# Performance work log

Hardware: AMD Instinct MI355X
Metric: run time of the kernel (lower is better)

Reference implementation:

```python
import jax, jax.numpy as jnp
import numpy as np

KERNEL_SIZE = 10
LEVELS = 4
PAD = (KERNEL_SIZE - 2) // 2  # 4


def _antireflect_pad(x, p):
    # antireflect: reflect around boundary value with sign flip: 2*edge - reflected interior
    left = 2.0 * x[..., :1] - x[..., 1:p + 1][..., ::-1]
    right = 2.0 * x[..., -1:] - x[..., -p - 1:-1][..., ::-1]
    return jnp.concatenate([left, x, right], axis=-1)


def _dwconv(x, kern, c):
    # depthwise grouped conv1d, stride 2, VALID (padding done explicitly)
    return jax.lax.conv_general_dilated(
        x, kern, window_strides=(2,), padding='VALID',
        feature_group_count=c, dimension_numbers=('NCH', 'OIH', 'NCH'))


def setup_inputs() -> dict:
    key = jax.random.key(0)
    k1, k2 = jax.random.split(key)
    signal = jax.random.normal(k1, (8, 64, 65536), dtype=jnp.float32)
    scaling_kernel = jax.random.normal(k2, (1, 1, KERNEL_SIZE), dtype=jnp.float32) * 0.3
    return {"signal": signal, "scaling_kernel": scaling_kernel}


def reference(signal, scaling_kernel):
    b, c, _ = signal.shape
    h = scaling_kernel  # [1,1,K]
    sign = (-1.0) ** jnp.arange(KERNEL_SIZE, dtype=signal.dtype)
    g = h[..., ::-1] * sign  # quadrature-mirror wavelet filter
    H = jnp.tile(h, (c, 1, 1))  # [C,1,K] depthwise kernels
    G = jnp.tile(g, (c, 1, 1))
    signals, details = [], []
    x = signal
    for _ in range(LEVELS):
        xp = _antireflect_pad(x, PAD)
        a = _dwconv(xp, H, c)  # approximation (normalize_approximation=False -> /1)
        d = _dwconv(xp, G, c)  # detail
        signals.append(a)
        details.append(d)
        x = jax.lax.stop_gradient(a)  # torch .detach() between levels
    return tuple(signals) + tuple(details)
```

## Files before the change

### kernel.cpp

```cpp
#include <hip/hip_runtime.h>

#define KS 10
#define NT 256
#define W  512

#define ARENA 1168

#define FENCE() asm volatile("s_waitcnt lgkmcnt(0)" ::: "memory")

struct OutPtrs { float* a[4]; float* d[4]; };

template<int EXT, int PADO, int OWN, bool TO_LDS>
__device__ __forceinline__ void wave_level(const float* __restrict__ sIn,
                                           float* __restrict__ sOut,
                                           const float* h,
                                           float* __restrict__ aRow,
                                           float* __restrict__ dRow,
                                           int obase, int lane)
{
    constexpr int ITERS = (EXT + 63) / 64;
#pragma unroll
    for (int i = 0; i < ITERS; ++i) {
        const int t = lane + 64 * i;
        if ((EXT % 64 == 0) || (t < EXT)) {
            float aa = 0.0f, dd = 0.0f;
#pragma unroll
            for (int k = 0; k < KS; ++k) {
                const float xv = sIn[2 * t + k];
                aa = fmaf(xv, h[k], aa);
                dd = fmaf(xv, (k & 1) ? -h[KS - 1 - k] : h[KS - 1 - k], dd);
            }
            if (TO_LDS) sOut[t] = aa;
            const int rel = t - PADO;
            if (rel >= 0 && rel < OWN) {
                aRow[obase + rel] = aa;
                dRow[obase + rel] = dd;
            }
        }
    }
}

__device__ __forceinline__ void patchL(float* s, int P, int lane) {
    if (lane < P) s[lane] = 2.0f * s[P] - s[2 * P - lane];
}
__device__ __forceinline__ void patchR(float* s, int P, int E, int lane) {
    if (lane < P) { const int t = E + 1 + lane; s[t] = 2.0f * s[E] - s[2 * E - t]; }
}

__global__ __launch_bounds__(NT) void dwt_wave_kernel(
    const float* __restrict__ x, const float* __restrict__ hptr, OutPtrs op, int L0)
{
    const int tid  = threadIdx.x;
    const int lane = tid & 63;
    const int wv   = tid >> 6;
    const int row  = blockIdx.y;
    const int nc   = L0 / W;
    const int c    = blockIdx.x * (NT / 64) + wv;
    const bool left  = (c == 0);
    const bool right = (c == nc - 1);

    __shared__ __align__(16) float arena[(NT / 64) * ARENA];
    float* sw  = arena + wv * ARENA;
    float* sx  = sw;
    float* sa1 = sx  + 632;
    float* sa2 = sa1 + 312;
    float* sa3 = sa2 + 152;

    float h[KS];
#pragma unroll
    for (int k = 0; k < KS; ++k) h[k] = hptr[k];

    const int L1 = L0 >> 1, L2 = L0 >> 2, L3 = L0 >> 3, L4 = L0 >> 4;
    float* a0row = op.a[0] + (size_t)row * L1;  float* d0row = op.d[0] + (size_t)row * L1;
    float* a1row = op.a[1] + (size_t)row * L2;  float* d1row = op.d[1] + (size_t)row * L2;
    float* a2row = op.a[2] + (size_t)row * L3;  float* d2row = op.d[2] + (size_t)row * L3;
    float* a3row = op.a[3] + (size_t)row * L4;  float* d3row = op.d[3] + (size_t)row * L4;

    const float* xr = x + (size_t)row * (size_t)L0;
    const int s0 = c * W - 60;
    {
        const int tlo = left ? 60 : 0;
        const int thi = right ? (W + 60) : (W + 120);
        const int nf4 = (thi - tlo) >> 2;
        const float4* src = reinterpret_cast<const float4*>(xr + s0 + tlo);
        float4* dst = reinterpret_cast<float4*>(sx + tlo);
        for (int j = lane; j < nf4; j += 64) dst[j] = src[j];
    }
    FENCE();
    if (left)  { patchL(sx, 60, lane);          FENCE(); }
    if (right) { patchR(sx, 60, W + 59, lane);  FENCE(); }

    wave_level<312, 28, 256, true >(sx,  sa1, h, a0row, d0row, c * 256, lane);
    FENCE();
    if (left)  { patchL(sa1, 28, lane);       FENCE(); }
    if (right) { patchR(sa1, 28, 283, lane);  FENCE(); }

    wave_level<152, 12, 128, true >(sa1, sa2, h, a1row, d1row, c * 128, lane);
    FENCE();
    if (left)  { patchL(sa2, 12, lane);       FENCE(); }
    if (right) { patchR(sa2, 12, 139, lane);  FENCE(); }

    wave_level< 72,  4,  64, true >(sa2, sa3, h, a2row, d2row, c * 64, lane);
    FENCE();
    if (left)  { patchL(sa3, 4, lane);        FENCE(); }
    if (right) { patchR(sa3, 4, 67, lane);    FENCE(); }

    wave_level< 32,  0,  32, false>(sa3, nullptr, h, a3row, d3row, c * 32, lane);
}

extern "C" void kernel_launch(void* const* d_in, const int* in_sizes, int n_in,
                              void* d_out, int out_size, void* d_ws, size_t ws_size,
                              hipStream_t stream) {
    (void)n_in; (void)d_ws; (void)ws_size; (void)out_size;

    const float* signal = (const float*)d_in[0];
    const float* h      = (const float*)d_in[1];
    float* out = (float*)d_out;

    const int L0 = 65536;
    const int R  = in_sizes[0] / L0;
    const int LEVELS = 4;

    size_t s_off[4], d_off[4];
    {
        size_t off = 0;
        int L = L0;
        for (int l = 0; l < LEVELS; ++l) { s_off[l] = off; off += (size_t)R * (size_t)(L >> 1); L >>= 1; }
        L = L0;
        for (int l = 0; l < LEVELS; ++l) { d_off[l] = off; off += (size_t)R * (size_t)(L >> 1); L >>= 1; }
    }

    OutPtrs op;
    for (int l = 0; l < LEVELS; ++l) { op.a[l] = out + s_off[l]; op.d[l] = out + d_off[l]; }

    dim3 grid(L0 / W / (NT / 64), R);
    dim3 block(NT);
    dwt_wave_kernel<<<grid, block, 0, stream>>>(signal, h, op, L0);
}
```

Measured before the change: 79.51 us.

## Compute level-1 directly from global registers, skipping input staging in LDS

Level 0 is now computed straight from per-lane float4 global loads into registers, with edge lanes building the antireflect values inline. Results go out as float4 stores and into LDS for level 1, so the input no longer passes through an LDS staging buffer. The level-1 halo values are recomputed from global memory by spare lanes. Later levels read LDS as float2 pairs. The smaller LDS arena may raise occupancy, at the cost of overlapping global reads and extra halo arithmetic.

```diff
diff --git a/kernel.cpp b/kernel.cpp
--- a/kernel.cpp
+++ b/kernel.cpp
@@ -4,7 +4,7 @@
 #define NT 256
 #define W  512
 
-#define ARENA 1168
+#define ARENA (312 + 152 + 72)
 
 #define FENCE() asm volatile("s_waitcnt lgkmcnt(0)" ::: "memory")
 
@@ -23,19 +23,22 @@
     for (int i = 0; i < ITERS; ++i) {
         const int t = lane + 64 * i;
         if ((EXT % 64 == 0) || (t < EXT)) {
+            const float2* p2 = reinterpret_cast<const float2*>(sIn);
+            float xin[10];
+#pragma unroll
+            for (int j = 0; j < 5; ++j) {
+                const float2 v = p2[t + j];
+                xin[2 * j] = v.x; xin[2 * j + 1] = v.y;
+            }
             float aa = 0.0f, dd = 0.0f;
 #pragma unroll
             for (int k = 0; k < KS; ++k) {
-                const float xv = sIn[2 * t + k];
-                aa = fmaf(xv, h[k], aa);
-                dd = fmaf(xv, (k & 1) ? -h[KS - 1 - k] : h[KS - 1 - k], dd);
+                aa = fmaf(xin[k], h[k], aa);
+                dd = fmaf(xin[k], (k & 1) ? -h[KS - 1 - k] : h[KS - 1 - k], dd);
             }
             if (TO_LDS) sOut[t] = aa;
             const int rel = t - PADO;
-            if (rel >= 0 && rel < OWN) {
-                aRow[obase + rel] = aa;
-                dRow[obase + rel] = dd;
-            }
+            if (rel >= 0 && rel < OWN) { aRow[obase + rel] = aa; dRow[obase + rel] = dd; }
         }
     }
 }
@@ -60,9 +63,7 @@
     const bool right = (c == nc - 1);
 
     __shared__ __align__(16) float arena[(NT / 64) * ARENA];
-    float* sw  = arena + wv * ARENA;
-    float* sx  = sw;
-    float* sa1 = sx  + 632;
+    float* sa1 = arena + wv * ARENA;
     float* sa2 = sa1 + 312;
     float* sa3 = sa2 + 152;
 
@@ -77,20 +78,61 @@
     float* a3row = op.a[3] + (size_t)row * L4;  float* d3row = op.d[3] + (size_t)row * L4;
 
     const float* xr = x + (size_t)row * (size_t)L0;
-    const int s0 = c * W - 60;
+    const int o1 = c * 256;
+
     {
-        const int tlo = left ? 60 : 0;
-        const int thi = right ? (W + 60) : (W + 120);
-        const int nf4 = (thi - tlo) >> 2;
-        const float4* src = reinterpret_cast<const float4*>(xr + s0 + tlo);
-        float4* dst = reinterpret_cast<float4*>(sx + tlo);
-        for (int j = lane; j < nf4; j += 64) dst[j] = src[j];
+        const int X = 2 * o1 + 8 * lane - 4;
+        float xv[16];
+        const bool eT = (left && lane == 0) || (right && lane == 63);
+        if (!eT) {
+            const float4* p = reinterpret_cast<const float4*>(xr + X);
+#pragma unroll
+            for (int q = 0; q < 4; ++q) {
+                const float4 v = p[q];
+                xv[4 * q] = v.x; xv[4 * q + 1] = v.y; xv[4 * q + 2] = v.z; xv[4 * q + 3] = v.w;
+            }
+        } else {
+#pragma unroll
+            for (int t = 0; t < 16; ++t) {
+                const int m = X + t;
+                float v;
+                if (m < 0)        v = 2.0f * xr[0]      - xr[-m];
+                else if (m >= L0) v = 2.0f * xr[L0 - 1] - xr[2 * L0 - 2 - m];
+                else              v = xr[m];
+                xv[t] = v;
+            }
+        }
+        float av[4], dv[4];
+#pragma unroll
+        for (int j = 0; j < 4; ++j) {
+            float aa = 0.0f, dd = 0.0f;
+#pragma unroll
+            for (int k = 0; k < KS; ++k) {
+                const float xx = xv[2 * j + k];
+                aa = fmaf(xx, h[k], aa);
+                dd = fmaf(xx, (k & 1) ? -h[KS - 1 - k] : h[KS - 1 - k], dd);
+            }
+            av[j] = aa; dv[j] = dd;
+        }
+        const int lane4 = 4 * lane;
+        *reinterpret_cast<float4*>(a0row + o1 + lane4) = make_float4(av[0], av[1], av[2], av[3]);
+        *reinterpret_cast<float4*>(d0row + o1 + lane4) = make_float4(dv[0], dv[1], dv[2], dv[3]);
+        *reinterpret_cast<float4*>(sa1 + 28 + lane4)   = make_float4(av[0], av[1], av[2], av[3]);
     }
-    FENCE();
-    if (left)  { patchL(sx, 60, lane);          FENCE(); }
-    if (right) { patchR(sx, 60, W + 59, lane);  FENCE(); }
 
-    wave_level<312, 28, 256, true >(sx,  sa1, h, a0row, d0row, c * 256, lane);
+    {
+        int ps = -1, v1p = 0;
+        if (lane < 28)                     { ps = lane;              v1p = o1 - 28 + lane; }
+        else if (lane >= 32 && lane < 60)  { ps = 284 + (lane - 32); v1p = o1 + 256 + (lane - 32); }
+        const bool skip = (left && lane < 32) || (right && lane >= 32);
+        if (ps >= 0 && !skip) {
+            const int xb = 2 * v1p - 4;
+            float acc = 0.0f;
+#pragma unroll
+            for (int k = 0; k < KS; ++k) acc = fmaf(xr[xb + k], h[k], acc);
+            sa1[ps] = acc;
+        }
+    }
     FENCE();
     if (left)  { patchL(sa1, 28, lane);       FENCE(); }
     if (right) { patchR(sa1, 28, 283, lane);  FENCE(); }
```

Result: faster. 75.31 us (-5.3%).
